# Kernel tuning notes

Hardware: AMD Instinct MI355X
Metric: run time of the kernel (lower is better)

Reference implementation:

```python
import jax, jax.numpy as jnp
import numpy as np

N = 100000
E = 1600000
F_IN = 128
HID = 64
N_CLS = 16


def gcn_conv(x, row, col, W, b, n_nodes):
    # x: [N, Fin]; row/col: [E+N] (self-loops already appended)
    h = x @ W  # [N, Fout]
    ones = jnp.ones(row.shape[0], dtype=x.dtype)
    deg = jax.ops.segment_sum(ones, col, num_segments=n_nodes)  # in-degree incl. self-loop
    dinv = jnp.where(deg > 0, jax.lax.rsqrt(deg), 0.0)
    norm = dinv[row] * dinv[col]  # [E+N]
    msg = h[row] * norm[:, None]  # gather + scale
    out = jax.ops.segment_sum(msg, col, num_segments=n_nodes)  # scatter-add
    return out + b


def setup_inputs() -> dict:
    key = jax.random.key(0)
    k1, k2, k3, k4, k5, k6 = jax.random.split(key, 6)
    x = jax.random.normal(k1, (N, F_IN), dtype=jnp.float32)
    edge_index = jax.random.randint(k2, (2, E), 0, N, dtype=jnp.int64)
    # Glorot-ish init for weights
    W1 = jax.random.normal(k3, (F_IN, HID), dtype=jnp.float32) / np.sqrt(F_IN)
    b1 = jnp.zeros((HID,), dtype=jnp.float32)
    W2 = jax.random.normal(k4, (HID, N_CLS), dtype=jnp.float32) / np.sqrt(HID)
    b2 = jnp.zeros((N_CLS,), dtype=jnp.float32)
    return {"x": x, "edge_index": edge_index, "W1": W1, "b1": b1, "W2": W2, "b2": b2}


def reference(x, edge_index, W1, b1, W2, b2):
    # Add self-loops (GCNConv default add_self_loops=True)
    loop = jnp.arange(N, dtype=edge_index.dtype)
    row = jnp.concatenate([edge_index[0], loop])
    col = jnp.concatenate([edge_index[1], loop])
    h = gcn_conv(x, row, col, W1, b1, N)
    h = jax.nn.relu(h)
    h = gcn_conv(h, row, col, W2, b2, N)
    return jax.nn.log_softmax(h, axis=1)
```

## Files before the change

### kernel.cpp

```cpp
#include <hip/hip_runtime.h>
#include <hip/hip_fp16.h>

#define F_IN 128
#define HID  64
#define NCLS 16
#define NPB  128
#define CAP  4096
#define CHUNK 4096
#define BINTHREADS 1024

typedef _Float16 half_t;
typedef __attribute__((ext_vector_type(8))) _Float16 half8;
typedef __attribute__((ext_vector_type(4))) float float4v;


__global__ __launch_bounds__(BINTHREADS) void phaseA(
    const int* __restrict__ row, const int* __restrict__ col,
    int* __restrict__ cursor, int* __restrict__ ebuf, int E, int NB,
    const float* __restrict__ W1, half_t* __restrict__ W1t, int nblkE)
{
    if ((int)blockIdx.x >= nblkE) {
        for (int i = threadIdx.x; i < F_IN * HID; i += BINTHREADS) {
            int k = i >> 6, n = i & 63;
            W1t[n * F_IN + k] = (half_t)W1[i];
        }
        return;
    }
    __shared__ int hist[1024], base[1024], off[1024];
    for (int i = threadIdx.x; i < NB; i += BINTHREADS) hist[i] = 0;
    int e0 = blockIdx.x * CHUNK + threadIdx.x * 4;
    int nv = min(max(E - e0, 0), 4);
    int4 c4 = make_int4(0, 0, 0, 0), r4 = make_int4(0, 0, 0, 0);
    if (nv == 4) {
        c4 = *(const int4*)&col[e0];
        r4 = *(const int4*)&row[e0];
    } else {
        if (nv > 0) { c4.x = col[e0 + 0]; r4.x = row[e0 + 0]; }
        if (nv > 1) { c4.y = col[e0 + 1]; r4.y = row[e0 + 1]; }
        if (nv > 2) { c4.z = col[e0 + 2]; r4.z = row[e0 + 2]; }
    }
    __syncthreads();
    if (nv > 0) atomicAdd(&hist[c4.x >> 7], 1);
    if (nv > 1) atomicAdd(&hist[c4.y >> 7], 1);
    if (nv > 2) atomicAdd(&hist[c4.z >> 7], 1);
    if (nv > 3) atomicAdd(&hist[c4.w >> 7], 1);
    __syncthreads();
    for (int i = threadIdx.x; i < NB; i += BINTHREADS) {
        int h = hist[i];
        base[i] = h ? (i * CAP + atomicAdd(&cursor[i], h)) : 0;
        off[i] = 0;
    }
    __syncthreads();
    if (nv > 0) { int b = c4.x >> 7; int p = base[b] + atomicAdd(&off[b], 1);
                  if (p < (b + 1) * CAP) ebuf[p] = (r4.x << 7) | (c4.x & (NPB - 1)); }
    if (nv > 1) { int b = c4.y >> 7; int p = base[b] + atomicAdd(&off[b], 1);
                  if (p < (b + 1) * CAP) ebuf[p] = (r4.y << 7) | (c4.y & (NPB - 1)); }
    if (nv > 2) { int b = c4.z >> 7; int p = base[b] + atomicAdd(&off[b], 1);
                  if (p < (b + 1) * CAP) ebuf[p] = (r4.z << 7) | (c4.z & (NPB - 1)); }
    if (nv > 3) { int b = c4.w >> 7; int p = base[b] + atomicAdd(&off[b], 1);
                  if (p < (b + 1) * CAP) ebuf[p] = (r4.w << 7) | (c4.w & (NPB - 1)); }
}


__global__ __launch_bounds__(256) void csr_gemm1(
    const int* __restrict__ ebuf, const int* __restrict__ cursor,
    const float* __restrict__ x, const half_t* __restrict__ W1t,
    int2* __restrict__ rsc, int* __restrict__ csr_row,
    __half* __restrict__ hs1, int N, int NG)
{
    __shared__ int hist[NPB];
    __shared__ float dv[NPB];
    int t = threadIdx.x;

    if ((int)blockIdx.x < NG) {
        int b = blockIdx.x;
        int node0 = b << 7;
        int ebase = b * CAP;
        int p[8];
        #pragma unroll
        for (int k = 0; k < 8; ++k) p[k] = ebuf[ebase + t + 256 * k];
        int cnt = min(cursor[b], CAP);
        if (t < NPB) hist[t] = 0;
        __syncthreads();
        #pragma unroll
        for (int k = 0; k < 8; ++k)
            if (t + 256 * k < cnt) atomicAdd(&hist[p[k] & (NPB - 1)], 1);
        if (cnt > 2048)
            for (int e = 2048 + t; e < cnt; e += 256)
                atomicAdd(&hist[ebuf[ebase + e] & (NPB - 1)], 1);
        __syncthreads();
        if (t < NPB) dv[t] = rsqrtf((float)hist[t] + 1.0f);
        __syncthreads();

        int wv = t >> 6, lane = t & 63;
        int l15 = lane & 15, quad = lane >> 4;
        int mbase = wv * 32;
        int r0 = min(node0 + mbase + l15, N - 1);
        int r1 = min(node0 + mbase + 16 + l15, N - 1);
        const float* x0 = x + (size_t)r0 * F_IN;
        const float* x1 = x + (size_t)r1 * F_IN;
        float4v acc[2][4];
        #pragma unroll
        for (int mt = 0; mt < 2; ++mt)
            #pragma unroll
            for (int j = 0; j < 4; ++j) acc[mt][j] = (float4v){0.f, 0.f, 0.f, 0.f};
        #pragma unroll
        for (int kb = 0; kb < 4; ++kb) {
            int off = kb * 32 + quad * 8;
            float4 fa = *(const float4*)&x0[off];
            float4 fb = *(const float4*)&x0[off + 4];
            float4 ga = *(const float4*)&x1[off];
            float4 gb = *(const float4*)&x1[off + 4];
            half8 a0 = {(half_t)fa.x, (half_t)fa.y, (half_t)fa.z, (half_t)fa.w,
                        (half_t)fb.x, (half_t)fb.y, (half_t)fb.z, (half_t)fb.w};
            half8 a1 = {(half_t)ga.x, (half_t)ga.y, (half_t)ga.z, (half_t)ga.w,
                        (half_t)gb.x, (half_t)gb.y, (half_t)gb.z, (half_t)gb.w};
            #pragma unroll
            for (int j = 0; j < 4; ++j) {
                half8 bv = *(const half8*)&W1t[(size_t)(j * 16 + l15) * F_IN + off];
                acc[0][j] = __builtin_amdgcn_mfma_f32_16x16x32_f16(a0, bv, acc[0][j], 0, 0, 0);
                acc[1][j] = __builtin_amdgcn_mfma_f32_16x16x32_f16(a1, bv, acc[1][j], 0, 0, 0);
            }
        }
        #pragma unroll
        for (int mt = 0; mt < 2; ++mt)
            #pragma unroll
            for (int j = 0; j < 4; ++j)
                #pragma unroll
                for (int r = 0; r < 4; ++r) {
                    int m = mbase + mt * 16 + quad * 4 + r;
                    int n = node0 + m;
                    if (n < N) hs1[(size_t)n * HID + j * 16 + l15] =
                        __float2half(acc[mt][j][r] * dv[m]);
                }
        return;
    }

    __shared__ int cur[NPB];
    __shared__ int wtot;
    int b = blockIdx.x - NG;
    int node0 = b << 7;
    int ebase = b * CAP;
    int p[8];
    #pragma unroll
    for (int k = 0; k < 8; ++k) p[k] = ebuf[ebase + t + 256 * k];
    int cnt = min(cursor[b], CAP);
    if (t < NPB) hist[t] = 0;
    __syncthreads();
    #pragma unroll
    for (int k = 0; k < 8; ++k)
        if (t + 256 * k < cnt) atomicAdd(&hist[p[k] & (NPB - 1)], 1);
    if (cnt > 2048)
        for (int e = 2048 + t; e < cnt; e += 256)
            atomicAdd(&hist[ebuf[ebase + e] & (NPB - 1)], 1);
    __syncthreads();
    int h = 0, incl = 0;
    if (t < NPB) {
        h = hist[t];
        incl = h;
        #pragma unroll
        for (int off = 1; off < 64; off <<= 1) {
            int u = __shfl_up(incl, off, 64);
            if ((t & 63) >= off) incl += u;
        }
        if (t == 63) wtot = incl;
    }
    __syncthreads();
    if (t < NPB) {
        if (t >= 64) incl += wtot;
        int start = ebase + incl - h;
        cur[t] = start;
        int n = node0 + t;
        if (n < N) rsc[n] = make_int2(start, h);
    }
    __syncthreads();
    #pragma unroll
    for (int k = 0; k < 8; ++k)
        if (t + 256 * k < cnt) {
            int pos = atomicAdd(&cur[p[k] & (NPB - 1)], 1);
            csr_row[pos] = p[k] >> 7;
        }
    if (cnt > 2048)
        for (int e = 2048 + t; e < cnt; e += 256) {
            int pp = ebuf[ebase + e];
            int pos = atomicAdd(&cur[pp & (NPB - 1)], 1);
            csr_row[pos] = pp >> 7;
        }
}


__global__ __launch_bounds__(256) void agg_l1(
    const __half* __restrict__ hs1, const int2* __restrict__ rsc,
    const int* __restrict__ csr, const float* __restrict__ b1,
    const float* __restrict__ W2, __half* __restrict__ h2s, int N)
{
    __shared__ float W2l[HID * NCLS];
    __shared__ float o1[32][65];
    for (int i = threadIdx.x; i < HID * NCLS; i += 256) W2l[i] = W2[i];
    __syncthreads();
    int w = threadIdx.x >> 6, lane = threadIdx.x & 63;
    int g = lane >> 3, gl = lane & 7;
    int rowi = w * 8 + g;
    int c = blockIdx.x * 32 + rowi;
    bool active = (c < N);
    int cc = active ? c : 0;
    int2 rc = rsc[cc];
    int e0 = rc.x, e1 = rc.x + rc.y;
    float dc = rsqrtf((float)rc.y + 1.0f);
    const half8* H = (const half8*)hs1;
    half8 sv = H[(size_t)cc * 8 + gl];
    float sum[8];
    #pragma unroll
    for (int k = 0; k < 8; ++k) sum[k] = (float)sv[k];
    int i = e0;
    for (; i + 8 <= e1; i += 8) {
        int id[8];
        #pragma unroll
        for (int s = 0; s < 8; ++s) id[s] = csr[i + s];
        half8 a[8];
        #pragma unroll
        for (int s = 0; s < 8; ++s) a[s] = H[(size_t)id[s] * 8 + gl];
        half8 t0 = a[0] + a[1];
        half8 t1 = a[2] + a[3];
        half8 t2 = a[4] + a[5];
        half8 t3 = a[6] + a[7];
        half8 u0 = t0 + t1;
        half8 u1 = t2 + t3;
        half8 v = u0 + u1;
        #pragma unroll
        for (int k = 0; k < 8; ++k) sum[k] += (float)v[k];
    }
    if (i < e1) {
        int e1m1 = e1 - 1;
        int id[8];
        #pragma unroll
        for (int s = 0; s < 8; ++s) id[s] = csr[min(i + s, e1m1)];
        half8 a[8];
        #pragma unroll
        for (int s = 0; s < 8; ++s) a[s] = H[(size_t)id[s] * 8 + gl];
        #pragma unroll
        for (int s = 0; s < 8; ++s) {
            float fm = (i + s < e1) ? 1.f : 0.f;
            #pragma unroll
            for (int k = 0; k < 8; ++k) sum[k] = fmaf(fm, (float)a[s][k], sum[k]);
        }
    }
    float4 bb0 = *(const float4*)&b1[gl * 8];
    float4 bb1 = *(const float4*)&b1[gl * 8 + 4];
    o1[rowi][gl * 8 + 0] = fmaxf(fmaf(dc, sum[0], bb0.x), 0.f);
    o1[rowi][gl * 8 + 1] = fmaxf(fmaf(dc, sum[1], bb0.y), 0.f);
    o1[rowi][gl * 8 + 2] = fmaxf(fmaf(dc, sum[2], bb0.z), 0.f);
    o1[rowi][gl * 8 + 3] = fmaxf(fmaf(dc, sum[3], bb0.w), 0.f);
    o1[rowi][gl * 8 + 4] = fmaxf(fmaf(dc, sum[4], bb1.x), 0.f);
    o1[rowi][gl * 8 + 5] = fmaxf(fmaf(dc, sum[5], bb1.y), 0.f);
    o1[rowi][gl * 8 + 6] = fmaxf(fmaf(dc, sum[6], bb1.z), 0.f);
    o1[rowi][gl * 8 + 7] = fmaxf(fmaf(dc, sum[7], bb1.w), 0.f);
    int j0 = gl * 2, j1 = gl * 2 + 1;
    float s0 = 0.f, s1 = 0.f;
    const float* orow = o1[rowi];
    #pragma unroll 8
    for (int k = 0; k < HID; ++k) {
        float ov = orow[k];
        s0 = fmaf(ov, W2l[k * NCLS + j0], s0);
        s1 = fmaf(ov, W2l[k * NCLS + j1], s1);
    }
    if (active) {
        __half2 hv;
        hv.x = __float2half(dc * s0);
        hv.y = __float2half(dc * s1);
        ((__half2*)h2s)[(size_t)c * 8 + gl] = hv;
    }
}


__global__ __launch_bounds__(256) void agg2_final(
    const __half* __restrict__ h2s, const int2* __restrict__ rsc,
    const int* __restrict__ csr, const float* __restrict__ b2,
    float* __restrict__ out, int N)
{
    int t = threadIdx.x;
    int w = t >> 6, lane = t & 63;
    int nw = lane >> 1, hl = lane & 1;
    int c = blockIdx.x * 128 + w * 32 + nw;
    bool active = (c < N);
    int cc = active ? c : 0;
    int2 rc = rsc[cc];
    int e0 = rc.x, e1 = rc.x + rc.y;
    float dcv = rsqrtf((float)rc.y + 1.0f);
    const half8* H = (const half8*)h2s;
    half8 sv = H[(size_t)cc * 2 + hl];
    float sum[8];
    #pragma unroll
    for (int k = 0; k < 8; ++k) sum[k] = (float)sv[k];
    int i = e0;
    for (; i + 8 <= e1; i += 8) {
        int id[8];
        #pragma unroll
        for (int s = 0; s < 8; ++s) id[s] = csr[i + s];
        half8 a[8];
        #pragma unroll
        for (int s = 0; s < 8; ++s) a[s] = H[(size_t)id[s] * 2 + hl];
        half8 t0 = a[0] + a[1];
        half8 t1 = a[2] + a[3];
        half8 t2 = a[4] + a[5];
        half8 t3 = a[6] + a[7];
        half8 v = (t0 + t1) + (t2 + t3);
        #pragma unroll
        for (int k = 0; k < 8; ++k) sum[k] += (float)v[k];
    }
    if (i < e1) {
        int e1m1 = e1 - 1;
        int id[8];
        #pragma unroll
        for (int s = 0; s < 8; ++s) id[s] = csr[min(i + s, e1m1)];
        half8 a[8];
        #pragma unroll
        for (int s = 0; s < 8; ++s) a[s] = H[(size_t)id[s] * 2 + hl];
        #pragma unroll
        for (int s = 0; s < 8; ++s) {
            float fm = (i + s < e1) ? 1.f : 0.f;
            #pragma unroll
            for (int k = 0; k < 8; ++k) sum[k] = fmaf(fm, (float)a[s][k], sum[k]);
        }
    }
    float4 bb0 = *(const float4*)&b2[hl * 8];
    float4 bb1 = *(const float4*)&b2[hl * 8 + 4];
    float v0 = fmaf(dcv, sum[0], bb0.x);
    float v1 = fmaf(dcv, sum[1], bb0.y);
    float v2 = fmaf(dcv, sum[2], bb0.z);
    float v3 = fmaf(dcv, sum[3], bb0.w);
    float v4 = fmaf(dcv, sum[4], bb1.x);
    float v5 = fmaf(dcv, sum[5], bb1.y);
    float v6 = fmaf(dcv, sum[6], bb1.z);
    float v7 = fmaf(dcv, sum[7], bb1.w);
    float mx = fmaxf(fmaxf(fmaxf(v0, v1), fmaxf(v2, v3)),
                     fmaxf(fmaxf(v4, v5), fmaxf(v6, v7)));
    mx = fmaxf(mx, __shfl_xor(mx, 1, 64));
    float s = __expf(v0 - mx) + __expf(v1 - mx) + __expf(v2 - mx) + __expf(v3 - mx)
            + __expf(v4 - mx) + __expf(v5 - mx) + __expf(v6 - mx) + __expf(v7 - mx);
    s += __shfl_xor(s, 1, 64);
    float lse = mx + __logf(s);
    if (active) {
        float* o = out + (size_t)c * NCLS + hl * 8;
        *(float4*)&o[0] = make_float4(v0 - lse, v1 - lse, v2 - lse, v3 - lse);
        *(float4*)&o[4] = make_float4(v4 - lse, v5 - lse, v6 - lse, v7 - lse);
    }
}


extern "C" void kernel_launch(void* const* d_in, const int* in_sizes, int n_in,
                              void* d_out, int out_size, void* d_ws, size_t ws_size,
                              hipStream_t stream) {
    const float* x  = (const float*)d_in[0];
    const int*   ei = (const int*)d_in[1];
    const float* W1 = (const float*)d_in[2];
    const float* b1 = (const float*)d_in[3];
    const float* W2 = (const float*)d_in[4];
    const float* b2 = (const float*)d_in[5];
    float* out = (float*)d_out;

    const int N = in_sizes[0] / F_IN;
    const int E = in_sizes[1] / 2;
    const int* row = ei;
    const int* col = ei + E;

    const int NB = (N + NPB - 1) / NPB;
    size_t Np  = ((size_t)N + 15) & ~(size_t)15;
    size_t NBp = ((size_t)NB + 15) & ~(size_t)15;
    size_t Rg  = (size_t)NB * CAP;

    char* p = (char*)d_ws;
    __half* hs1     = (__half*)p;  p += Np * HID * 2;
    __half* h2s     = (__half*)p;  p += Np * NCLS * 2;
    half_t* W1t     = (half_t*)p;  p += (size_t)F_IN * HID * 2;
    int2*   rsc     = (int2*)p;    p += Np * 8;
    int*    csr_row = (int*)p;     p += Rg * 4;
    int*    ebuf    = (int*)p;     p += Rg * 4;
    int*    cursor  = (int*)p;     p += NBp * 4;

    int nblkE = (E + CHUNK - 1) / CHUNK;

    hipMemsetAsync(cursor, 0, NBp * sizeof(int), stream);
    phaseA<<<nblkE + 1, BINTHREADS, 0, stream>>>(row, col, cursor, ebuf, E, NB, W1, W1t, nblkE);
    csr_gemm1<<<2 * NB, 256, 0, stream>>>(ebuf, cursor, x, W1t, rsc, csr_row, hs1, N, NB);
    agg_l1<<<(N + 31) / 32, 256, 0, stream>>>(hs1, rsc, csr_row, b1, W2, h2s, N);
    agg2_final<<<(N + 127) / 128, 256, 0, stream>>>(h2s, rsc, csr_row, b2, out, N);
}
```

Measured before the change: 182.0 us.

## Build CSR via global per-node degree atomics and direct scatter

Replaces the two-level bucketed binning (block-local histogram into a per-bucket ebuf, then a per-bucket local sort) with a global per-node in-degree count using global atomics, a per-bucket prefix scan kernel, and a direct atomic scatter of row indices into csr_row. This removes the intermediate ebuf write and re-read and the packed-index encoding. The GEMM now reads degrees from the global array. It adds one kernel launch and relies on millions of contended global atomics on a 100K-entry array instead of LDS atomics. The CSR order within each node also becomes nondeterministic.

```diff
diff --git a/kernel.cpp b/kernel.cpp
--- a/kernel.cpp
+++ b/kernel.cpp
@@ -7,185 +7,150 @@
 #define NPB  128
 #define CAP  4096
 #define CHUNK 4096
-#define BINTHREADS 1024
 
 typedef _Float16 half_t;
 typedef __attribute__((ext_vector_type(8))) _Float16 half8;
 typedef __attribute__((ext_vector_type(4))) float float4v;
 
 
-__global__ __launch_bounds__(BINTHREADS) void phaseA(
-    const int* __restrict__ row, const int* __restrict__ col,
-    int* __restrict__ cursor, int* __restrict__ ebuf, int E, int NB,
-    const float* __restrict__ W1, half_t* __restrict__ W1t, int nblkE)
-{
-    if ((int)blockIdx.x >= nblkE) {
-        for (int i = threadIdx.x; i < F_IN * HID; i += BINTHREADS) {
+__global__ __launch_bounds__(256) void deg_w1(
+    const int* __restrict__ col, const float* __restrict__ W1,
+    int* __restrict__ deg, half_t* __restrict__ W1t, int E, int nch)
+{
+    if ((int)blockIdx.x >= nch) {
+        for (int i = threadIdx.x; i < F_IN * HID; i += 256) {
             int k = i >> 6, n = i & 63;
             W1t[n * F_IN + k] = (half_t)W1[i];
         }
         return;
     }
-    __shared__ int hist[1024], base[1024], off[1024];
-    for (int i = threadIdx.x; i < NB; i += BINTHREADS) hist[i] = 0;
-    int e0 = blockIdx.x * CHUNK + threadIdx.x * 4;
-    int nv = min(max(E - e0, 0), 4);
-    int4 c4 = make_int4(0, 0, 0, 0), r4 = make_int4(0, 0, 0, 0);
-    if (nv == 4) {
-        c4 = *(const int4*)&col[e0];
-        r4 = *(const int4*)&row[e0];
-    } else {
-        if (nv > 0) { c4.x = col[e0 + 0]; r4.x = row[e0 + 0]; }
-        if (nv > 1) { c4.y = col[e0 + 1]; r4.y = row[e0 + 1]; }
-        if (nv > 2) { c4.z = col[e0 + 2]; r4.z = row[e0 + 2]; }
-    }
+    int base = blockIdx.x * CHUNK;
+    #pragma unroll
+    for (int j = 0; j < 4; ++j) {
+        int ej = base + j * (CHUNK / 4) + threadIdx.x * 4;
+        if (ej + 4 <= E) {
+            int4 c4 = *(const int4*)&col[ej];
+            atomicAdd(&deg[c4.x], 1);
+            atomicAdd(&deg[c4.y], 1);
+            atomicAdd(&deg[c4.z], 1);
+            atomicAdd(&deg[c4.w], 1);
+        } else {
+            for (int q = ej; q < E; ++q) atomicAdd(&deg[col[q]], 1);
+        }
+    }
+}
+
+
+__global__ __launch_bounds__(128) void scan_init(
+    const int* __restrict__ deg, int2* __restrict__ rsc,
+    int* __restrict__ curg, int N)
+{
+    __shared__ int wtot;
+    int b = blockIdx.x, t = threadIdx.x;
+    int n = (b << 7) + t;
+    int h = (n < N) ? deg[n] : 0;
+    int incl = h;
+    #pragma unroll
+    for (int off = 1; off < 64; off <<= 1) {
+        int u = __shfl_up(incl, off, 64);
+        if ((t & 63) >= off) incl += u;
+    }
+    if (t == 63) wtot = incl;
     __syncthreads();
-    if (nv > 0) atomicAdd(&hist[c4.x >> 7], 1);
-    if (nv > 1) atomicAdd(&hist[c4.y >> 7], 1);
-    if (nv > 2) atomicAdd(&hist[c4.z >> 7], 1);
-    if (nv > 3) atomicAdd(&hist[c4.w >> 7], 1);
+    if (t >= 64) incl += wtot;
+    int start = b * CAP + incl - h;
+    if (n < N) {
+        rsc[n] = make_int2(start, h);
+        curg[n] = start;
+    }
+}
+
+
+__global__ __launch_bounds__(256) void scatter_gemm(
+    const int* __restrict__ row, const int* __restrict__ col,
+    int* __restrict__ curg, int* __restrict__ csr_row,
+    const float* __restrict__ x, const half_t* __restrict__ W1t,
+    const int* __restrict__ deg, __half* __restrict__ hs1,
+    int N, int E, int nch)
+{
+    int t = threadIdx.x;
+    if ((int)blockIdx.x < nch) {
+        int base = blockIdx.x * CHUNK;
+        #pragma unroll
+        for (int j = 0; j < 4; ++j) {
+            int ej = base + j * (CHUNK / 4) + t * 4;
+            if (ej + 4 <= E) {
+                int4 c4 = *(const int4*)&col[ej];
+                int4 r4 = *(const int4*)&row[ej];
+                int p0 = atomicAdd(&curg[c4.x], 1);
+                if (p0 < ((c4.x >> 7) + 1) * CAP) csr_row[p0] = r4.x;
+                int p1 = atomicAdd(&curg[c4.y], 1);
+                if (p1 < ((c4.y >> 7) + 1) * CAP) csr_row[p1] = r4.y;
+                int p2 = atomicAdd(&curg[c4.z], 1);
+                if (p2 < ((c4.z >> 7) + 1) * CAP) csr_row[p2] = r4.z;
+                int p3 = atomicAdd(&curg[c4.w], 1);
+                if (p3 < ((c4.w >> 7) + 1) * CAP) csr_row[p3] = r4.w;
+            } else {
+                for (int q = ej; q < E; ++q) {
+                    int c = col[q];
+                    int p = atomicAdd(&curg[c], 1);
+                    if (p < ((c >> 7) + 1) * CAP) csr_row[p] = row[q];
+                }
+            }
+        }
+        return;
+    }
+
+    __shared__ float dv[NPB];
+    int b = blockIdx.x - nch;
+    int node0 = b << 7;
+    if (t < NPB) {
+        int n = node0 + t;
+        dv[t] = rsqrtf((float)((n < N) ? deg[n] : 0) + 1.0f);
+    }
     __syncthreads();
-    for (int i = threadIdx.x; i < NB; i += BINTHREADS) {
-        int h = hist[i];
-        base[i] = h ? (i * CAP + atomicAdd(&cursor[i], h)) : 0;
-        off[i] = 0;
-    }
-    __syncthreads();
-    if (nv > 0) { int b = c4.x >> 7; int p = base[b] + atomicAdd(&off[b], 1);
-                  if (p < (b + 1) * CAP) ebuf[p] = (r4.x << 7) | (c4.x & (NPB - 1)); }
-    if (nv > 1) { int b = c4.y >> 7; int p = base[b] + atomicAdd(&off[b], 1);
-                  if (p < (b + 1) * CAP) ebuf[p] = (r4.y << 7) | (c4.y & (NPB - 1)); }
-    if (nv > 2) { int b = c4.z >> 7; int p = base[b] + atomicAdd(&off[b], 1);
-                  if (p < (b + 1) * CAP) ebuf[p] = (r4.z << 7) | (c4.z & (NPB - 1)); }
-    if (nv > 3) { int b = c4.w >> 7; int p = base[b] + atomicAdd(&off[b], 1);
-                  if (p < (b + 1) * CAP) ebuf[p] = (r4.w << 7) | (c4.w & (NPB - 1)); }
-}
-
-
-__global__ __launch_bounds__(256) void csr_gemm1(
-    const int* __restrict__ ebuf, const int* __restrict__ cursor,
-    const float* __restrict__ x, const half_t* __restrict__ W1t,
-    int2* __restrict__ rsc, int* __restrict__ csr_row,
-    __half* __restrict__ hs1, int N, int NG)
-{
-    __shared__ int hist[NPB];
-    __shared__ float dv[NPB];
-    int t = threadIdx.x;
-
-    if ((int)blockIdx.x < NG) {
-        int b = blockIdx.x;
-        int node0 = b << 7;
-        int ebase = b * CAP;
-        int p[8];
-        #pragma unroll
-        for (int k = 0; k < 8; ++k) p[k] = ebuf[ebase + t + 256 * k];
-        int cnt = min(cursor[b], CAP);
-        if (t < NPB) hist[t] = 0;
-        __syncthreads();
-        #pragma unroll
-        for (int k = 0; k < 8; ++k)
-            if (t + 256 * k < cnt) atomicAdd(&hist[p[k] & (NPB - 1)], 1);
-        if (cnt > 2048)
-            for (int e = 2048 + t; e < cnt; e += 256)
-                atomicAdd(&hist[ebuf[ebase + e] & (NPB - 1)], 1);
-        __syncthreads();
-        if (t < NPB) dv[t] = rsqrtf((float)hist[t] + 1.0f);
-        __syncthreads();
-
-        int wv = t >> 6, lane = t & 63;
-        int l15 = lane & 15, quad = lane >> 4;
-        int mbase = wv * 32;
-        int r0 = min(node0 + mbase + l15, N - 1);
-        int r1 = min(node0 + mbase + 16 + l15, N - 1);
-        const float* x0 = x + (size_t)r0 * F_IN;
-        const float* x1 = x + (size_t)r1 * F_IN;
-        float4v acc[2][4];
-        #pragma unroll
-        for (int mt = 0; mt < 2; ++mt)
+
+    int wv = t >> 6, lane = t & 63;
+    int l15 = lane & 15, quad = lane >> 4;
+    int mbase = wv * 32;
+    int r0 = min(node0 + mbase + l15, N - 1);
+    int r1 = min(node0 + mbase + 16 + l15, N - 1);
+    const float* x0 = x + (size_t)r0 * F_IN;
+    const float* x1 = x + (size_t)r1 * F_IN;
+    float4v acc[2][4];
+    #pragma unroll
+    for (int mt = 0; mt < 2; ++mt)
+        #pragma unroll
+        for (int j = 0; j < 4; ++j) acc[mt][j] = (float4v){0.f, 0.f, 0.f, 0.f};
+    #pragma unroll
+    for (int kb = 0; kb < 4; ++kb) {
+        int off = kb * 32 + quad * 8;
+        float4 fa = *(const float4*)&x0[off];
+        float4 fb = *(const float4*)&x0[off + 4];
+        float4 ga = *(const float4*)&x1[off];
+        float4 gb = *(const float4*)&x1[off + 4];
+        half8 a0 = {(half_t)fa.x, (half_t)fa.y, (half_t)fa.z, (half_t)fa.w,
+                    (half_t)fb.x, (half_t)fb.y, (half_t)fb.z, (half_t)fb.w};
+        half8 a1 = {(half_t)ga.x, (half_t)ga.y, (half_t)ga.z, (half_t)ga.w,
+                    (half_t)gb.x, (half_t)gb.y, (half_t)gb.z, (half_t)gb.w};
+        #pragma unroll
+        for (int j = 0; j < 4; ++j) {
+            half8 bv = *(const half8*)&W1t[(size_t)(j * 16 + l15) * F_IN + off];
+            acc[0][j] = __builtin_amdgcn_mfma_f32_16x16x32_f16(a0, bv, acc[0][j], 0, 0, 0);
+            acc[1][j] = __builtin_amdgcn_mfma_f32_16x16x32_f16(a1, bv, acc[1][j], 0, 0, 0);
+        }
+    }
+    #pragma unroll
+    for (int mt = 0; mt < 2; ++mt)
+        #pragma unroll
+        for (int j = 0; j < 4; ++j)
             #pragma unroll
-            for (int j = 0; j < 4; ++j) acc[mt][j] = (float4v){0.f, 0.f, 0.f, 0.f};
-        #pragma unroll
-        for (int kb = 0; kb < 4; ++kb) {
-            int off = kb * 32 + quad * 8;
-            float4 fa = *(const float4*)&x0[off];
-            float4 fb = *(const float4*)&x0[off + 4];
-            float4 ga = *(const float4*)&x1[off];
-            float4 gb = *(const float4*)&x1[off + 4];
-            half8 a0 = {(half_t)fa.x, (half_t)fa.y, (half_t)fa.z, (half_t)fa.w,
-                        (half_t)fb.x, (half_t)fb.y, (half_t)fb.z, (half_t)fb.w};
-            half8 a1 = {(half_t)ga.x, (half_t)ga.y, (half_t)ga.z, (half_t)ga.w,
-                        (half_t)gb.x, (half_t)gb.y, (half_t)gb.z, (half_t)gb.w};
-            #pragma unroll
-            for (int j = 0; j < 4; ++j) {
-                half8 bv = *(const half8*)&W1t[(size_t)(j * 16 + l15) * F_IN + off];
-                acc[0][j] = __builtin_amdgcn_mfma_f32_16x16x32_f16(a0, bv, acc[0][j], 0, 0, 0);
-                acc[1][j] = __builtin_amdgcn_mfma_f32_16x16x32_f16(a1, bv, acc[1][j], 0, 0, 0);
+            for (int r = 0; r < 4; ++r) {
+                int m = mbase + mt * 16 + quad * 4 + r;
+                int n = node0 + m;
+                if (n < N) hs1[(size_t)n * HID + j * 16 + l15] =
+                    __float2half(acc[mt][j][r] * dv[m]);
             }
-        }
-        #pragma unroll
-        for (int mt = 0; mt < 2; ++mt)
-            #pragma unroll
-            for (int j = 0; j < 4; ++j)
-                #pragma unroll
-                for (int r = 0; r < 4; ++r) {
-                    int m = mbase + mt * 16 + quad * 4 + r;
-                    int n = node0 + m;
-                    if (n < N) hs1[(size_t)n * HID + j * 16 + l15] =
-                        __float2half(acc[mt][j][r] * dv[m]);
-                }
-        return;
-    }
-
-    __shared__ int cur[NPB];
-    __shared__ int wtot;
-    int b = blockIdx.x - NG;
-    int node0 = b << 7;
-    int ebase = b * CAP;
-    int p[8];
-    #pragma unroll
-    for (int k = 0; k < 8; ++k) p[k] = ebuf[ebase + t + 256 * k];
-    int cnt = min(cursor[b], CAP);
-    if (t < NPB) hist[t] = 0;
-    __syncthreads();
-    #pragma unroll
-    for (int k = 0; k < 8; ++k)
-        if (t + 256 * k < cnt) atomicAdd(&hist[p[k] & (NPB - 1)], 1);
-    if (cnt > 2048)
-        for (int e = 2048 + t; e < cnt; e += 256)
-            atomicAdd(&hist[ebuf[ebase + e] & (NPB - 1)], 1);
-    __syncthreads();
-    int h = 0, incl = 0;
-    if (t < NPB) {
-        h = hist[t];
-        incl = h;
-        #pragma unroll
-        for (int off = 1; off < 64; off <<= 1) {
-            int u = __shfl_up(incl, off, 64);
-            if ((t & 63) >= off) incl += u;
-        }
-        if (t == 63) wtot = incl;
-    }
-    __syncthreads();
-    if (t < NPB) {
-        if (t >= 64) incl += wtot;
-        int start = ebase + incl - h;
-        cur[t] = start;
-        int n = node0 + t;
-        if (n < N) rsc[n] = make_int2(start, h);
-    }
-    __syncthreads();
-    #pragma unroll
-    for (int k = 0; k < 8; ++k)
-        if (t + 256 * k < cnt) {
-            int pos = atomicAdd(&cur[p[k] & (NPB - 1)], 1);
-            csr_row[pos] = p[k] >> 7;
-        }
-    if (cnt > 2048)
-        for (int e = 2048 + t; e < cnt; e += 256) {
-            int pp = ebuf[ebase + e];
-            int pos = atomicAdd(&cur[pp & (NPB - 1)], 1);
-            csr_row[pos] = pp >> 7;
-        }
 }
 
 
@@ -224,9 +189,7 @@
         half8 t1 = a[2] + a[3];
         half8 t2 = a[4] + a[5];
         half8 t3 = a[6] + a[7];
-        half8 u0 = t0 + t1;
-        half8 u1 = t2 + t3;
-        half8 v = u0 + u1;
+        half8 v = (t0 + t1) + (t2 + t3);
         #pragma unroll
         for (int k = 0; k < 8; ++k) sum[k] += (float)v[k];
     }
@@ -366,7 +329,6 @@
 
     const int NB = (N + NPB - 1) / NPB;
     size_t Np  = ((size_t)N + 15) & ~(size_t)15;
-    size_t NBp = ((size_t)NB + 15) & ~(size_t)15;
     size_t Rg  = (size_t)NB * CAP;
 
     char* p = (char*)d_ws;
@@ -375,14 +337,16 @@
     half_t* W1t     = (half_t*)p;  p += (size_t)F_IN * HID * 2;
     int2*   rsc     = (int2*)p;    p += Np * 8;
     int*    csr_row = (int*)p;     p += Rg * 4;
-    int*    ebuf    = (int*)p;     p += Rg * 4;
-    int*    cursor  = (int*)p;     p += NBp * 4;
-
-    int nblkE = (E + CHUNK - 1) / CHUNK;
-
-    hipMemsetAsync(cursor, 0, NBp * sizeof(int), stream);
-    phaseA<<<nblkE + 1, BINTHREADS, 0, stream>>>(row, col, cursor, ebuf, E, NB, W1, W1t, nblkE);
-    csr_gemm1<<<2 * NB, 256, 0, stream>>>(ebuf, cursor, x, W1t, rsc, csr_row, hs1, N, NB);
+    int*    deg     = (int*)p;     p += Np * 4;
+    int*    curg    = (int*)p;     p += Np * 4;
+
+    int nch = (E + CHUNK - 1) / CHUNK;
+
+    hipMemsetAsync(deg, 0, Np * sizeof(int), stream);
+    deg_w1<<<nch + 1, 256, 0, stream>>>(col, W1, deg, W1t, E, nch);
+    scan_init<<<NB, 128, 0, stream>>>(deg, rsc, curg, N);
+    scatter_gemm<<<nch + NB, 256, 0, stream>>>(row, col, curg, csr_row, x, W1t,
+                                               deg, hs1, N, E, nch);
     agg_l1<<<(N + 31) / 32, 256, 0, stream>>>(hs1, rsc, csr_row, b1, W2, h2s, N);
     agg2_final<<<(N + 127) / 128, 256, 0, stream>>>(h2s, rsc, csr_row, b2, out, N);
 }
```

New measurement: 286.1 us. 57.2% more time.

## Overlap X·W1 GEMM with edge binning and apply degree scaling afterwards

Applied to the files above, without the earlier changes.

Moves the dense X·W1 GEMM into the binning kernel so it runs concurrently with edge bucketing, since it no longer depends on degrees. Each GEMM block transposes W1 into padded shared memory instead of reading a pre-transposed global copy. The rsqrt degree scaling is applied in a read-modify-write pass over hs1 inside the CSR-build kernel. Binning blocks drop from 1024 to 256 threads, with each thread now handling four int4 groups. The tradeoff is an extra read and write of hs1 and a per-block conversion of W1.

```diff
diff --git a/kernel.cpp b/kernel.cpp
--- a/kernel.cpp
+++ b/kernel.cpp
@@ -7,140 +7,141 @@
 #define NPB  128
 #define CAP  4096
 #define CHUNK 4096
-#define BINTHREADS 1024
+#define W1PAD 136
 
 typedef _Float16 half_t;
 typedef __attribute__((ext_vector_type(8))) _Float16 half8;
 typedef __attribute__((ext_vector_type(4))) float float4v;
 
 
-__global__ __launch_bounds__(BINTHREADS) void phaseA(
+__global__ __launch_bounds__(256) void bin_gemm(
     const int* __restrict__ row, const int* __restrict__ col,
-    int* __restrict__ cursor, int* __restrict__ ebuf, int E, int NB,
-    const float* __restrict__ W1, half_t* __restrict__ W1t, int nblkE)
+    const float* __restrict__ x, const float* __restrict__ W1,
+    int* __restrict__ cursor, int* __restrict__ ebuf,
+    __half* __restrict__ hs1, int N, int E, int NB, int nbin)
 {
-    if ((int)blockIdx.x >= nblkE) {
-        for (int i = threadIdx.x; i < F_IN * HID; i += BINTHREADS) {
-            int k = i >> 6, n = i & 63;
-            W1t[n * F_IN + k] = (half_t)W1[i];
+    __shared__ __align__(16) char smem[17408];
+    int t = threadIdx.x;
+
+    if ((int)blockIdx.x < nbin) {
+        int* hist = (int*)smem;
+        int* base = (int*)smem + 1024;
+        int* off  = (int*)smem + 2048;
+        for (int i = t; i < NB; i += 256) hist[i] = 0;
+        int base_e = blockIdx.x * CHUNK;
+        int4 c4[4], r4[4];
+        int nv[4];
+        #pragma unroll
+        for (int j = 0; j < 4; ++j) {
+            int ej = base_e + j * 1024 + t * 4;
+            int n = min(max(E - ej, 0), 4);
+            nv[j] = n;
+            c4[j] = make_int4(0, 0, 0, 0); r4[j] = make_int4(0, 0, 0, 0);
+            if (n == 4) {
+                c4[j] = *(const int4*)&col[ej];
+                r4[j] = *(const int4*)&row[ej];
+            } else {
+                if (n > 0) { c4[j].x = col[ej + 0]; r4[j].x = row[ej + 0]; }
+                if (n > 1) { c4[j].y = col[ej + 1]; r4[j].y = row[ej + 1]; }
+                if (n > 2) { c4[j].z = col[ej + 2]; r4[j].z = row[ej + 2]; }
+            }
+        }
+        __syncthreads();
+        #pragma unroll
+        for (int j = 0; j < 4; ++j) {
+            if (nv[j] > 0) atomicAdd(&hist[c4[j].x >> 7], 1);
+            if (nv[j] > 1) atomicAdd(&hist[c4[j].y >> 7], 1);
+            if (nv[j] > 2) atomicAdd(&hist[c4[j].z >> 7], 1);
+            if (nv[j] > 3) atomicAdd(&hist[c4[j].w >> 7], 1);
+        }
+        __syncthreads();
+        for (int i = t; i < NB; i += 256) {
+            int h = hist[i];
+            base[i] = h ? (i * CAP + atomicAdd(&cursor[i], h)) : 0;
+            off[i] = 0;
+        }
+        __syncthreads();
+        #pragma unroll
+        for (int j = 0; j < 4; ++j) {
+            if (nv[j] > 0) { int b = c4[j].x >> 7; int p = base[b] + atomicAdd(&off[b], 1);
+                             if (p < (b + 1) * CAP) ebuf[p] = (r4[j].x << 7) | (c4[j].x & (NPB - 1)); }
+            if (nv[j] > 1) { int b = c4[j].y >> 7; int p = base[b] + atomicAdd(&off[b], 1);
+                             if (p < (b + 1) * CAP) ebuf[p] = (r4[j].y << 7) | (c4[j].y & (NPB - 1)); }
+            if (nv[j] > 2) { int b = c4[j].z >> 7; int p = base[b] + atomicAdd(&off[b], 1);
+                             if (p < (b + 1) * CAP) ebuf[p] = (r4[j].z << 7) | (c4[j].z & (NPB - 1)); }
+            if (nv[j] > 3) { int b = c4[j].w >> 7; int p = base[b] + atomicAdd(&off[b], 1);
+                             if (p < (b + 1) * CAP) ebuf[p] = (r4[j].w << 7) | (c4[j].w & (NPB - 1)); }
         }
         return;
     }
-    __shared__ int hist[1024], base[1024], off[1024];
-    for (int i = threadIdx.x; i < NB; i += BINTHREADS) hist[i] = 0;
-    int e0 = blockIdx.x * CHUNK + threadIdx.x * 4;
-    int nv = min(max(E - e0, 0), 4);
-    int4 c4 = make_int4(0, 0, 0, 0), r4 = make_int4(0, 0, 0, 0);
-    if (nv == 4) {
-        c4 = *(const int4*)&col[e0];
-        r4 = *(const int4*)&row[e0];
-    } else {
-        if (nv > 0) { c4.x = col[e0 + 0]; r4.x = row[e0 + 0]; }
-        if (nv > 1) { c4.y = col[e0 + 1]; r4.y = row[e0 + 1]; }
-        if (nv > 2) { c4.z = col[e0 + 2]; r4.z = row[e0 + 2]; }
-    }
-    __syncthreads();
-    if (nv > 0) atomicAdd(&hist[c4.x >> 7], 1);
-    if (nv > 1) atomicAdd(&hist[c4.y >> 7], 1);
-    if (nv > 2) atomicAdd(&hist[c4.z >> 7], 1);
-    if (nv > 3) atomicAdd(&hist[c4.w >> 7], 1);
-    __syncthreads();
-    for (int i = threadIdx.x; i < NB; i += BINTHREADS) {
-        int h = hist[i];
-        base[i] = h ? (i * CAP + atomicAdd(&cursor[i], h)) : 0;
-        off[i] = 0;
-    }
-    __syncthreads();
-    if (nv > 0) { int b = c4.x >> 7; int p = base[b] + atomicAdd(&off[b], 1);
-                  if (p < (b + 1) * CAP) ebuf[p] = (r4.x << 7) | (c4.x & (NPB - 1)); }
-    if (nv > 1) { int b = c4.y >> 7; int p = base[b] + atomicAdd(&off[b], 1);
-                  if (p < (b + 1) * CAP) ebuf[p] = (r4.y << 7) | (c4.y & (NPB - 1)); }
-    if (nv > 2) { int b = c4.z >> 7; int p = base[b] + atomicAdd(&off[b], 1);
-                  if (p < (b + 1) * CAP) ebuf[p] = (r4.z << 7) | (c4.z & (NPB - 1)); }
-    if (nv > 3) { int b = c4.w >> 7; int p = base[b] + atomicAdd(&off[b], 1);
-                  if (p < (b + 1) * CAP) ebuf[p] = (r4.w << 7) | (c4.w & (NPB - 1)); }
+
+    half_t* W1l = (half_t*)smem;
+    for (int i = t; i < F_IN * HID; i += 256) {
+        int k = i >> 6, n = i & 63;
+        W1l[n * W1PAD + k] = (half_t)W1[i];
+    }
+    __syncthreads();
+
+    int b = blockIdx.x - nbin;
+    int node0 = b << 7;
+    int wv = t >> 6, lane = t & 63;
+    int l15 = lane & 15, quad = lane >> 4;
+    int mbase = wv * 32;
+    int r0 = min(node0 + mbase + l15, N - 1);
+    int r1 = min(node0 + mbase + 16 + l15, N - 1);
+    const float* x0 = x + (size_t)r0 * F_IN;
+    const float* x1 = x + (size_t)r1 * F_IN;
+    float4v acc[2][4];
+    #pragma unroll
+    for (int mt = 0; mt < 2; ++mt)
+        #pragma unroll
+        for (int j = 0; j < 4; ++j) acc[mt][j] = (float4v){0.f, 0.f, 0.f, 0.f};
+    #pragma unroll
+    for (int kb = 0; kb < 4; ++kb) {
+        int off = kb * 32 + quad * 8;
+        float4 fa = *(const float4*)&x0[off];
+        float4 fb = *(const float4*)&x0[off + 4];
+        float4 ga = *(const float4*)&x1[off];
+        float4 gb = *(const float4*)&x1[off + 4];
+        half8 a0 = {(half_t)fa.x, (half_t)fa.y, (half_t)fa.z, (half_t)fa.w,
+                    (half_t)fb.x, (half_t)fb.y, (half_t)fb.z, (half_t)fb.w};
+        half8 a1 = {(half_t)ga.x, (half_t)ga.y, (half_t)ga.z, (half_t)ga.w,
+                    (half_t)gb.x, (half_t)gb.y, (half_t)gb.z, (half_t)gb.w};
+        #pragma unroll
+        for (int j = 0; j < 4; ++j) {
+            half8 bv = *(const half8*)&W1l[(j * 16 + l15) * W1PAD + off];
+            acc[0][j] = __builtin_amdgcn_mfma_f32_16x16x32_f16(a0, bv, acc[0][j], 0, 0, 0);
+            acc[1][j] = __builtin_amdgcn_mfma_f32_16x16x32_f16(a1, bv, acc[1][j], 0, 0, 0);
+        }
+    }
+    #pragma unroll
+    for (int mt = 0; mt < 2; ++mt)
+        #pragma unroll
+        for (int j = 0; j < 4; ++j)
+            #pragma unroll
+            for (int r = 0; r < 4; ++r) {
+                int m = mbase + mt * 16 + quad * 4 + r;
+                int nn = node0 + m;
+                if (nn < N) hs1[(size_t)nn * HID + j * 16 + l15] =
+                    __float2half(acc[mt][j][r]);
+            }
 }
 
 
-__global__ __launch_bounds__(256) void csr_gemm1(
+__global__ __launch_bounds__(256) void csr_scale(
     const int* __restrict__ ebuf, const int* __restrict__ cursor,
-    const float* __restrict__ x, const half_t* __restrict__ W1t,
     int2* __restrict__ rsc, int* __restrict__ csr_row,
-    __half* __restrict__ hs1, int N, int NG)
+    __half* __restrict__ hs1, int N)
 {
     __shared__ int hist[NPB];
     __shared__ float dv[NPB];
-    int t = threadIdx.x;
-
-    if ((int)blockIdx.x < NG) {
-        int b = blockIdx.x;
-        int node0 = b << 7;
-        int ebase = b * CAP;
-        int p[8];
-        #pragma unroll
-        for (int k = 0; k < 8; ++k) p[k] = ebuf[ebase + t + 256 * k];
-        int cnt = min(cursor[b], CAP);
-        if (t < NPB) hist[t] = 0;
-        __syncthreads();
-        #pragma unroll
-        for (int k = 0; k < 8; ++k)
-            if (t + 256 * k < cnt) atomicAdd(&hist[p[k] & (NPB - 1)], 1);
-        if (cnt > 2048)
-            for (int e = 2048 + t; e < cnt; e += 256)
-                atomicAdd(&hist[ebuf[ebase + e] & (NPB - 1)], 1);
-        __syncthreads();
-        if (t < NPB) dv[t] = rsqrtf((float)hist[t] + 1.0f);
-        __syncthreads();
-
-        int wv = t >> 6, lane = t & 63;
-        int l15 = lane & 15, quad = lane >> 4;
-        int mbase = wv * 32;
-        int r0 = min(node0 + mbase + l15, N - 1);
-        int r1 = min(node0 + mbase + 16 + l15, N - 1);
-        const float* x0 = x + (size_t)r0 * F_IN;
-        const float* x1 = x + (size_t)r1 * F_IN;
-        float4v acc[2][4];
-        #pragma unroll
-        for (int mt = 0; mt < 2; ++mt)
-            #pragma unroll
-            for (int j = 0; j < 4; ++j) acc[mt][j] = (float4v){0.f, 0.f, 0.f, 0.f};
-        #pragma unroll
-        for (int kb = 0; kb < 4; ++kb) {
-            int off = kb * 32 + quad * 8;
-            float4 fa = *(const float4*)&x0[off];
-            float4 fb = *(const float4*)&x0[off + 4];
-            float4 ga = *(const float4*)&x1[off];
-            float4 gb = *(const float4*)&x1[off + 4];
-            half8 a0 = {(half_t)fa.x, (half_t)fa.y, (half_t)fa.z, (half_t)fa.w,
-                        (half_t)fb.x, (half_t)fb.y, (half_t)fb.z, (half_t)fb.w};
-            half8 a1 = {(half_t)ga.x, (half_t)ga.y, (half_t)ga.z, (half_t)ga.w,
-                        (half_t)gb.x, (half_t)gb.y, (half_t)gb.z, (half_t)gb.w};
-            #pragma unroll
-            for (int j = 0; j < 4; ++j) {
-                half8 bv = *(const half8*)&W1t[(size_t)(j * 16 + l15) * F_IN + off];
-                acc[0][j] = __builtin_amdgcn_mfma_f32_16x16x32_f16(a0, bv, acc[0][j], 0, 0, 0);
-                acc[1][j] = __builtin_amdgcn_mfma_f32_16x16x32_f16(a1, bv, acc[1][j], 0, 0, 0);
-            }
-        }
-        #pragma unroll
-        for (int mt = 0; mt < 2; ++mt)
-            #pragma unroll
-            for (int j = 0; j < 4; ++j)
-                #pragma unroll
-                for (int r = 0; r < 4; ++r) {
-                    int m = mbase + mt * 16 + quad * 4 + r;
-                    int n = node0 + m;
-                    if (n < N) hs1[(size_t)n * HID + j * 16 + l15] =
-                        __float2half(acc[mt][j][r] * dv[m]);
-                }
-        return;
-    }
-
     __shared__ int cur[NPB];
     __shared__ int wtot;
-    int b = blockIdx.x - NG;
+    int t = threadIdx.x;
+    int b = blockIdx.x;
     int node0 = b << 7;
     int ebase = b * CAP;
+
     int p[8];
     #pragma unroll
     for (int k = 0; k < 8; ++k) p[k] = ebuf[ebase + t + 256 * k];
@@ -154,6 +155,7 @@
         for (int e = 2048 + t; e < cnt; e += 256)
             atomicAdd(&hist[ebuf[ebase + e] & (NPB - 1)], 1);
     __syncthreads();
+
     int h = 0, incl = 0;
     if (t < NPB) {
         h = hist[t];
@@ -164,6 +166,7 @@
             if ((t & 63) >= off) incl += u;
         }
         if (t == 63) wtot = incl;
+        dv[t] = rsqrtf((float)h + 1.0f);
     }
     __syncthreads();
     if (t < NPB) {
@@ -174,6 +177,7 @@
         if (n < N) rsc[n] = make_int2(start, h);
     }
     __syncthreads();
+
     #pragma unroll
     for (int k = 0; k < 8; ++k)
         if (t + 256 * k < cnt) {
@@ -186,6 +190,19 @@
             int pos = atomicAdd(&cur[pp & (NPB - 1)], 1);
             csr_row[pos] = pp >> 7;
         }
+
+    half8* H = (half8*)hs1;
+    for (int i = t; i < 1024; i += 256) {
+        int r = i >> 3, s8 = i & 7;
+        int n = node0 + r;
+        if (n < N) {
+            half8 v = H[(size_t)n * 8 + s8];
+            float d = dv[r];
+            #pragma unroll
+            for (int k = 0; k < 8; ++k) v[k] = (half_t)((float)v[k] * d);
+            H[(size_t)n * 8 + s8] = v;
+        }
+    }
 }
 
 
@@ -224,9 +241,7 @@
         half8 t1 = a[2] + a[3];
         half8 t2 = a[4] + a[5];
         half8 t3 = a[6] + a[7];
-        half8 u0 = t0 + t1;
-        half8 u1 = t2 + t3;
-        half8 v = u0 + u1;
+        half8 v = (t0 + t1) + (t2 + t3);
         #pragma unroll
         for (int k = 0; k < 8; ++k) sum[k] += (float)v[k];
     }
@@ -372,17 +387,17 @@
     char* p = (char*)d_ws;
     __half* hs1     = (__half*)p;  p += Np * HID * 2;
     __half* h2s     = (__half*)p;  p += Np * NCLS * 2;
-    half_t* W1t     = (half_t*)p;  p += (size_t)F_IN * HID * 2;
     int2*   rsc     = (int2*)p;    p += Np * 8;
     int*    csr_row = (int*)p;     p += Rg * 4;
     int*    ebuf    = (int*)p;     p += Rg * 4;
     int*    cursor  = (int*)p;     p += NBp * 4;
 
-    int nblkE = (E + CHUNK - 1) / CHUNK;
+    int nbin = (E + CHUNK - 1) / CHUNK;
 
     hipMemsetAsync(cursor, 0, NBp * sizeof(int), stream);
-    phaseA<<<nblkE + 1, BINTHREADS, 0, stream>>>(row, col, cursor, ebuf, E, NB, W1, W1t, nblkE);
-    csr_gemm1<<<2 * NB, 256, 0, stream>>>(ebuf, cursor, x, W1t, rsc, csr_row, hs1, N, NB);
+    bin_gemm<<<nbin + NB, 256, 0, stream>>>(row, col, x, W1, cursor, ebuf,
+                                            hs1, N, E, NB, nbin);
+    csr_scale<<<NB, 256, 0, stream>>>(ebuf, cursor, rsc, csr_row, hs1, N);
     agg_l1<<<(N + 31) / 32, 256, 0, stream>>>(hs1, rsc, csr_row, b1, W2, h2s, N);
     agg2_final<<<(N + 127) / 128, 256, 0, stream>>>(h2s, rsc, csr_row, b2, out, N);
 }
```

Result: slower. 190.1 us (+4.4%).
